# Kernel optimization log

Hardware: AMD Instinct MI355X
Metric: run time of the kernel (lower is better)

The kernel has to match this reference:

```python
import jax, jax.numpy as jnp
import numpy as np

B, S, H, I = 2, 1024, 1024, 4096
G, E = 4, 4
NE = G * E
CAP = 1024


def setup_inputs() -> dict:
    key = jax.random.key(0)
    ks = jax.random.split(key, 6)
    return {
        "hidden_states": jax.random.normal(ks[0], (B, S, H), jnp.float32),
        "group_router_w": jax.random.normal(ks[1], (G, H), jnp.float32) * 0.02,
        "expert_router_w": jax.random.normal(ks[2], (G, E, H), jnp.float32) * 0.02,
        "gate_w": jax.random.normal(ks[3], (NE, I, H), jnp.float32) * 0.02,
        "up_w": jax.random.normal(ks[4], (NE, I, H), jnp.float32) * 0.02,
        "down_w": jax.random.normal(ks[5], (NE, H, I), jnp.float32) * 0.02,
    }


def _forward(x, gw, erw, Wg, Wu, Wd):
    b, s, h = x.shape
    T = b * s
    xf = x.reshape(T, h)
    # level 1: group routing (fp32 softmax, top-2 groups)
    group_logits = xf @ gw.T                                        # [T,G]
    group_probs = jax.nn.softmax(group_logits.astype(jnp.float32), axis=-1)
    top_gp, top_gi = jax.lax.top_k(group_probs, 2)                  # [T,2]
    # level 2: per-group expert routing (top-1 expert within group)
    expert_logits = jnp.einsum('th,geh->tge', xf, erw)              # [T,G,E]
    expert_probs = jax.nn.softmax(expert_logits.astype(jnp.float32), axis=-1)
    e_idx = jnp.argmax(expert_probs, axis=-1)                       # [T,G]
    e_prob = jnp.max(expert_probs, axis=-1)                         # [T,G]
    sel_e = jnp.take_along_axis(e_idx, top_gi, axis=1)              # [T,2]
    sel_p = jnp.take_along_axis(e_prob, top_gi, axis=1)             # [T,2]
    eid = (top_gi * E + sel_e).reshape(-1)                          # [2T] global expert id
    wgt = (top_gp * sel_p).reshape(-1)                              # [2T] combine weight
    x2 = jnp.repeat(xf, 2, axis=0)                                  # [2T,H], slot-major per token
    # capacity-based dispatch: position within expert via cumsum of one-hot
    onehot = jax.nn.one_hot(eid, NE, dtype=jnp.int32)               # [2T,NE]
    pos = (jnp.cumsum(onehot, axis=0) * onehot).sum(axis=1) - 1     # [2T]
    keep = pos < CAP
    pos_c = jnp.where(keep, pos, CAP)                               # overflow -> dummy slot
    buf = jnp.zeros((NE, CAP + 1, h), x.dtype).at[eid, pos_c].set(x2)
    # grouped-GEMM gated FFN (SwiGLU) over all experts at once
    gate = jax.nn.silu(jnp.einsum('ech,eih->eci', buf, Wg))
    up = jnp.einsum('ech,eih->eci', buf, Wu)
    yexp = jnp.einsum('eci,ehi->ech', gate * up, Wd)                # [NE,CAP+1,H]
    # combine: gather back and weight; dropped tokens get zero weight
    y = yexp[eid, pos_c] * jnp.where(keep, wgt, 0.0)[:, None].astype(x.dtype)
    out = (y[0::2] + y[1::2]).reshape(b, s, h)
    aux_loss = jnp.zeros((), jnp.float32)  # aux-loss accumulation truncated in source; initialized to 0
    return out, aux_loss


def reference(hidden_states, group_router_w, expert_router_w, gate_w, up_w, down_w):
    return _forward(hidden_states, group_router_w, expert_router_w, gate_w, up_w, down_w)
```

## Files before the change

kernel.cpp:

```cpp
#include <hip/hip_runtime.h>
#include <hip/hip_bf16.h>

typedef float f32x4 __attribute__((ext_vector_type(4)));
typedef __bf16 bf16x8 __attribute__((ext_vector_type(8)));

#define H 1024
#define II 4096
#define NE 16
#define CAP 1024
#define NTOK 2048
#define NSLOT 4096

__global__ __launch_bounds__(256) void k_route(
    const float* __restrict__ x, const float* __restrict__ gw,
    const float* __restrict__ erw, int* __restrict__ eid,
    float* __restrict__ wgt) {
  int t = blockIdx.x * 4 + (threadIdx.x >> 6);
  int lane = threadIdx.x & 63;
  const float* xr = x + (size_t)t * H;
  double acc[20];
#pragma unroll
  for (int j = 0; j < 20; j++) acc[j] = 0.0;
  for (int it = 0; it < 16; ++it) {
    int h = it * 64 + lane;
    float xv = xr[h];
#pragma unroll
    for (int g = 0; g < 4; ++g) acc[g] += (double)xv * (double)gw[g * H + h];
#pragma unroll
    for (int j = 0; j < 16; ++j)
      acc[4 + j] += (double)xv * (double)erw[j * H + h];
  }
#pragma unroll
  for (int j = 0; j < 20; ++j) {
    double v = acc[j];
#pragma unroll
    for (int o = 32; o > 0; o >>= 1) v += __shfl_down(v, o, 64);
    acc[j] = v;
  }
  if (lane == 0) {
    float gl[4];
#pragma unroll
    for (int g = 0; g < 4; g++) gl[g] = (float)acc[g];
    int g1 = 0;
#pragma unroll
    for (int g = 1; g < 4; g++)
      if (gl[g] > gl[g1]) g1 = g;
    int g2 = (g1 == 0) ? 1 : 0;
#pragma unroll
    for (int g = 0; g < 4; g++)
      if (g != g1 && gl[g] > gl[g2]) g2 = g;
    float gm = fmaxf(fmaxf(gl[0], gl[1]), fmaxf(gl[2], gl[3]));
    float s = 0.f;
#pragma unroll
    for (int g = 0; g < 4; g++) s += expf(gl[g] - gm);
    float p[2] = {expf(gl[g1] - gm) / s, expf(gl[g2] - gm) / s};
    int gs[2] = {g1, g2};
#pragma unroll
    for (int k = 0; k < 2; k++) {
      int g = gs[k];
      float el[4];
#pragma unroll
      for (int e2 = 0; e2 < 4; e2++) el[e2] = (float)acc[4 + g * 4 + e2];
      int eb = 0;
#pragma unroll
      for (int e2 = 1; e2 < 4; e2++)
        if (el[e2] > el[eb]) eb = e2;
      float es = 0.f;
#pragma unroll
      for (int e2 = 0; e2 < 4; e2++) es += expf(el[e2] - el[eb]);
      eid[2 * t + k] = g * 4 + eb;
      wgt[2 * t + k] = p[k] * (1.f / es);
    }
  }
}

__global__ __launch_bounds__(1024) void k_scan(const int* __restrict__ eid,
                                               int* __restrict__ perm,
                                               int* __restrict__ cnt,
                                               int* __restrict__ kept) {
  int wid = threadIdx.x >> 6;
  int lane = threadIdx.x & 63;
  int base = 0;
  for (int it = 0; it < 64; ++it) {
    int slot = it * 64 + lane;
    int e = eid[slot];
    unsigned long long m = __ballot(e == wid);
    if (e == wid) {
      int pos = base + __popcll(m & ((1ull << lane) - 1ull));
      if (pos < CAP) {
        perm[wid * CAP + pos] = slot;
        kept[slot] = 1;
      } else {
        kept[slot] = 0;
      }
    }
    base += __popcll(m);
  }
  if (lane == 0) cnt[wid] = (base < CAP) ? base : CAP;
}

__global__ __launch_bounds__(256) void k_cvtx(const float* __restrict__ x,
                                              __bf16* __restrict__ xb) {
  size_t i = ((size_t)blockIdx.x * 256 + threadIdx.x) * 8;
  f32x4 a = *(const f32x4*)(x + i);
  f32x4 b = *(const f32x4*)(x + i + 4);
  bf16x8 o;
#pragma unroll
  for (int j = 0; j < 4; j++) {
    o[j] = (__bf16)a[j];
    o[j + 4] = (__bf16)b[j];
  }
  *(bf16x8*)(xb + i) = o;
}

#define FENCE_BAR()                                    \
  asm volatile("s_waitcnt lgkmcnt(0)" ::: "memory");   \
  __builtin_amdgcn_sched_barrier(0);                   \
  __builtin_amdgcn_s_barrier();

__global__ __launch_bounds__(256, 2) void k_gateup(
    const __bf16* __restrict__ xb, const float* __restrict__ Wg,
    const float* __restrict__ Wu, const int* __restrict__ perm,
    const int* __restrict__ cnt, __bf16* __restrict__ act) {
  __shared__ __bf16 As[2][128 * 64];
  __shared__ __bf16 Gs[2][64 * 64];
  __shared__ __bf16 Us[2][64 * 64];
  __shared__ int slotArr[128];
  const int e = blockIdx.z, nt = blockIdx.x, rt = blockIdx.y;
  const int ce = cnt[e];
  if (rt * 128 >= ce) return;
  const int tid = threadIdx.x, lane = tid & 63, wid = tid >> 6;
  if (tid < 128) {
    int ridx = rt * 128 + tid;
    slotArr[tid] = perm[e * CAP + (ridx < ce ? ridx : 0)];
  }
  __syncthreads();
  const int srow = tid >> 3;
  const int sch = tid & 7;
  const __bf16* pA[4];
  int wrA[4];
#pragma unroll
  for (int q = 0; q < 4; q++) {
    int r = q * 32 + srow;
    pA[q] = xb + (size_t)(slotArr[r] >> 1) * H + sch * 8;
    wrA[q] = r * 64 + (sch ^ (r & 7)) * 8;
  }
  const size_t ew = (size_t)e * II * H + (size_t)(nt * 64) * H;
  const float* pG[2];
  const float* pU[2];
  int wrW[2];
#pragma unroll
  for (int q = 0; q < 2; q++) {
    int r = q * 32 + srow;
    pG[q] = Wg + ew + (size_t)r * H + sch * 8;
    pU[q] = Wu + ew + (size_t)r * H + sch * 8;
    wrW[q] = r * 64 + (sch ^ (r & 7)) * 8;
  }
  const int wm = wid >> 1, wn = wid & 1;
  f32x4 accG[4][2], accU[4][2];
#pragma unroll
  for (int m = 0; m < 4; m++)
#pragma unroll
    for (int n = 0; n < 2; n++)
#pragma unroll
      for (int i = 0; i < 4; i++) {
        accG[m][n][i] = 0.f;
        accU[m][n][i] = 0.f;
      }
  bf16x8 a0[4], a1[4];
  f32x4 g00[2], g01[2], u00[2], u01[2];
  f32x4 g10[2], g11[2], u10[2], u11[2];

#define GU_LOADS(AS, G0, G1, U0, U1, T)                                    \
  {                                                                        \
    const int ko = (T) * 64;                                               \
    _Pragma("unroll") for (int q = 0; q < 4; q++)                          \
        AS[q] = *(const bf16x8*)(pA[q] + ko);                              \
    _Pragma("unroll") for (int q = 0; q < 2; q++) {                        \
      G0[q] = *(const f32x4*)(pG[q] + ko);                                 \
      G1[q] = *(const f32x4*)(pG[q] + ko + 4);                             \
      U0[q] = *(const f32x4*)(pU[q] + ko);                                 \
      U1[q] = *(const f32x4*)(pU[q] + ko + 4);                             \
    }                                                                      \
  }
#define GU_WRITE(BUF, AS, G0, G1, U0, U1)                                  \
  {                                                                        \
    _Pragma("unroll") for (int q = 0; q < 4; q++)                          \
        *(bf16x8*)&As[BUF][wrA[q]] = AS[q];                                \
    _Pragma("unroll") for (int q = 0; q < 2; q++) {                        \
      bf16x8 fg, fu;                                                       \
      _Pragma("unroll") for (int i = 0; i < 4; i++) {                      \
        fg[i] = (__bf16)G0[q][i];                                          \
        fg[i + 4] = (__bf16)G1[q][i];                                      \
        fu[i] = (__bf16)U0[q][i];                                          \
        fu[i + 4] = (__bf16)U1[q][i];                                      \
      }                                                                    \
      *(bf16x8*)&Gs[BUF][wrW[q]] = fg;                                     \
      *(bf16x8*)&Us[BUF][wrW[q]] = fu;                                     \
    }                                                                      \
  }
#define GU_COMPUTE(BUF)                                                    \
  {                                                                        \
    _Pragma("unroll") for (int kk = 0; kk < 2; ++kk) {                     \
      bf16x8 aF[4], gF[2], uF[2];                                          \
      _Pragma("unroll") for (int m = 0; m < 4; m++) {                      \
        int r = wm * 64 + m * 16 + (lane & 15);                            \
        int c = (kk * 4 + (lane >> 4)) ^ (r & 7);                          \
        aF[m] = *(const bf16x8*)&As[BUF][r * 64 + c * 8];                  \
      }                                                                    \
      _Pragma("unroll") for (int n = 0; n < 2; n++) {                      \
        int rg = wn * 32 + n * 16 + (lane & 15);                           \
        int c = (kk * 4 + (lane >> 4)) ^ (rg & 7);                         \
        gF[n] = *(const bf16x8*)&Gs[BUF][rg * 64 + c * 8];                 \
        uF[n] = *(const bf16x8*)&Us[BUF][rg * 64 + c * 8];                 \
      }                                                                    \
      _Pragma("unroll") for (int m = 0; m < 4; m++)                        \
          _Pragma("unroll") for (int n = 0; n < 2; n++) {                  \
        accG[m][n] = __builtin_amdgcn_mfma_f32_16x16x32_bf16(              \
            aF[m], gF[n], accG[m][n], 0, 0, 0);                            \
        accU[m][n] = __builtin_amdgcn_mfma_f32_16x16x32_bf16(              \
            aF[m], uF[n], accU[m][n], 0, 0, 0);                            \
      }                                                                    \
    }                                                                      \
  }

  GU_LOADS(a0, g00, g01, u00, u01, 0);
  GU_LOADS(a1, g10, g11, u10, u11, 1);
  GU_WRITE(0, a0, g00, g01, u00, u01);
  FENCE_BAR();
  for (int tt = 0; tt < 8; ++tt) {
    const int t0 = 2 * tt;
    if (t0 + 2 < 16) GU_LOADS(a0, g00, g01, u00, u01, t0 + 2);
    GU_COMPUTE(0);
    GU_WRITE(1, a1, g10, g11, u10, u11);
    FENCE_BAR();
    const int t1 = t0 + 1;
    if (t1 + 2 < 16) GU_LOADS(a1, g10, g11, u10, u11, t1 + 2);
    GU_COMPUTE(1);
    if (t1 + 1 < 16) {
      GU_WRITE(0, a0, g00, g01, u00, u01);
      FENCE_BAR();
    }
  }
  const int colB = nt * 64 + wn * 32;
#pragma unroll
  for (int m = 0; m < 4; m++)
#pragma unroll
    for (int n = 0; n < 2; n++)
#pragma unroll
      for (int i = 0; i < 4; i++) {
        int row = wm * 64 + m * 16 + (lane >> 4) * 4 + i;
        if (rt * 128 + row < ce) {
          int slot = slotArr[row];
          float g = accG[m][n][i];
          float u = accU[m][n][i];
          float a = (g / (1.f + __expf(-g))) * u;
          act[(size_t)slot * II + colB + n * 16 + (lane & 15)] = (__bf16)a;
        }
      }
}

__global__ __launch_bounds__(256, 2) void k_down(
    const __bf16* __restrict__ act, const float* __restrict__ Wd,
    const int* __restrict__ perm, const int* __restrict__ cnt,
    const float* __restrict__ wgt, float* __restrict__ y) {
  __shared__ __bf16 As[2][128 * 64];
  __shared__ __bf16 Ws[2][64 * 64];
  __shared__ int slotArr[128];
  const int e = blockIdx.z, nt = blockIdx.x, rt = blockIdx.y;
  const int ce = cnt[e];
  if (rt * 128 >= ce) return;
  const int tid = threadIdx.x, lane = tid & 63, wid = tid >> 6;
  if (tid < 128) {
    int ridx = rt * 128 + tid;
    slotArr[tid] = perm[e * CAP + (ridx < ce ? ridx : 0)];
  }
  __syncthreads();
  const int srow = tid >> 3;
  const int sch = tid & 7;
  const __bf16* pA[4];
  int wrA[4];
#pragma unroll
  for (int q = 0; q < 4; q++) {
    int r = q * 32 + srow;
    pA[q] = act + (size_t)slotArr[r] * II + sch * 8;
    wrA[q] = r * 64 + (sch ^ (r & 7)) * 8;
  }
  const float* pW[2];
  int wrW[2];
#pragma unroll
  for (int q = 0; q < 2; q++) {
    int r = q * 32 + srow;
    pW[q] = Wd + (size_t)e * H * II + (size_t)(nt * 64 + r) * II + sch * 8;
    wrW[q] = r * 64 + (sch ^ (r & 7)) * 8;
  }
  const int wm = wid >> 1, wn = wid & 1;
  f32x4 acc[4][2];
#pragma unroll
  for (int m = 0; m < 4; m++)
#pragma unroll
    for (int n = 0; n < 2; n++)
#pragma unroll
      for (int i = 0; i < 4; i++) acc[m][n][i] = 0.f;
  bf16x8 a0[4], a1[4];
  f32x4 w00[2], w01[2], w10[2], w11[2];

#define DN_LOADS(AS, W0, W1, T)                                            \
  {                                                                        \
    const int ko = (T) * 64;                                               \
    _Pragma("unroll") for (int q = 0; q < 4; q++)                          \
        AS[q] = *(const bf16x8*)(pA[q] + ko);                              \
    _Pragma("unroll") for (int q = 0; q < 2; q++) {                        \
      W0[q] = *(const f32x4*)(pW[q] + ko);                                 \
      W1[q] = *(const f32x4*)(pW[q] + ko + 4);                             \
    }                                                                      \
  }
#define DN_WRITE(BUF, AS, W0, W1)                                          \
  {                                                                        \
    _Pragma("unroll") for (int q = 0; q < 4; q++)                          \
        *(bf16x8*)&As[BUF][wrA[q]] = AS[q];                                \
    _Pragma("unroll") for (int q = 0; q < 2; q++) {                        \
      bf16x8 fw;                                                           \
      _Pragma("unroll") for (int i = 0; i < 4; i++) {                      \
        fw[i] = (__bf16)W0[q][i];                                          \
        fw[i + 4] = (__bf16)W1[q][i];                                      \
      }                                                                    \
      *(bf16x8*)&Ws[BUF][wrW[q]] = fw;                                     \
    }                                                                      \
  }
#define DN_COMPUTE(BUF)                                                    \
  {                                                                        \
    _Pragma("unroll") for (int kk = 0; kk < 2; ++kk) {                     \
      bf16x8 aF[4], wF[2];                                                 \
      _Pragma("unroll") for (int m = 0; m < 4; m++) {                      \
        int r = wm * 64 + m * 16 + (lane & 15);                            \
        int c = (kk * 4 + (lane >> 4)) ^ (r & 7);                          \
        aF[m] = *(const bf16x8*)&As[BUF][r * 64 + c * 8];                  \
      }                                                                    \
      _Pragma("unroll") for (int n = 0; n < 2; n++) {                      \
        int rw = wn * 32 + n * 16 + (lane & 15);                           \
        int c = (kk * 4 + (lane >> 4)) ^ (rw & 7);                         \
        wF[n] = *(const bf16x8*)&Ws[BUF][rw * 64 + c * 8];                 \
      }                                                                    \
      _Pragma("unroll") for (int m = 0; m < 4; m++)                        \
          _Pragma("unroll") for (int n = 0; n < 2; n++)                    \
              acc[m][n] = __builtin_amdgcn_mfma_f32_16x16x32_bf16(         \
                  aF[m], wF[n], acc[m][n], 0, 0, 0);                       \
    }                                                                      \
  }

  DN_LOADS(a0, w00, w01, 0);
  DN_LOADS(a1, w10, w11, 1);
  DN_WRITE(0, a0, w00, w01);
  FENCE_BAR();
  for (int tt = 0; tt < 32; ++tt) {
    const int t0 = 2 * tt;
    if (t0 + 2 < 64) DN_LOADS(a0, w00, w01, t0 + 2);
    DN_COMPUTE(0);
    DN_WRITE(1, a1, w10, w11);
    FENCE_BAR();
    const int t1 = t0 + 1;
    if (t1 + 2 < 64) DN_LOADS(a1, w10, w11, t1 + 2);
    DN_COMPUTE(1);
    if (t1 + 1 < 64) {
      DN_WRITE(0, a0, w00, w01);
      FENCE_BAR();
    }
  }
  const int colB = nt * 64 + wn * 32;
#pragma unroll
  for (int m = 0; m < 4; m++)
#pragma unroll
    for (int n = 0; n < 2; n++)
#pragma unroll
      for (int i = 0; i < 4; i++) {
        int row = wm * 64 + m * 16 + (lane >> 4) * 4 + i;
        if (rt * 128 + row < ce) {
          int slot = slotArr[row];
          y[(size_t)slot * H + colB + n * 16 + (lane & 15)] =
              wgt[slot] * acc[m][n][i];
        }
      }
}

__global__ __launch_bounds__(256) void k_combine(const float* __restrict__ y,
                                                 const int* __restrict__ kept,
                                                 float* __restrict__ out) {
  int t = blockIdx.x, tid = threadIdx.x;
  const f32x4* y0 = (const f32x4*)(y + (size_t)(2 * t) * H);
  const f32x4* y1 = (const f32x4*)(y + (size_t)(2 * t + 1) * H);
  f32x4 a, b;
#pragma unroll
  for (int i = 0; i < 4; i++) {
    a[i] = 0.f;
    b[i] = 0.f;
  }
  if (kept[2 * t]) a = y0[tid];
  if (kept[2 * t + 1]) b = y1[tid];
  ((f32x4*)out)[(size_t)t * 256 + tid] = a + b;
  if (t == 0 && tid == 0) out[(size_t)NTOK * H] = 0.f;
}

extern "C" void kernel_launch(void* const* d_in, const int* in_sizes, int n_in,
                              void* d_out, int out_size, void* d_ws,
                              size_t ws_size, hipStream_t stream) {
  const float* x = (const float*)d_in[0];
  const float* gw = (const float*)d_in[1];
  const float* erw = (const float*)d_in[2];
  const float* Wg = (const float*)d_in[3];
  const float* Wu = (const float*)d_in[4];
  const float* Wd = (const float*)d_in[5];
  float* out = (float*)d_out;
  char* ws = (char*)d_ws;
  int* eid = (int*)(ws);
  float* wgt = (float*)(ws + (16 << 10));
  int* kept = (int*)(ws + (32 << 10));
  int* cnt = (int*)(ws + (48 << 10));
  int* perm = (int*)(ws + (64 << 10));
  __bf16* act = (__bf16*)(ws + (128 << 10));
  float* yb = (float*)(ws + (128 << 10) + (size_t)NSLOT * II * 2);
  __bf16* xb = (__bf16*)(ws + (128 << 10) + (size_t)NSLOT * II * 2 +
                         (size_t)NSLOT * H * 4);

  k_route<<<NTOK / 4, 256, 0, stream>>>(x, gw, erw, eid, wgt);
  k_scan<<<1, 1024, 0, stream>>>(eid, perm, cnt, kept);
  k_cvtx<<<NTOK * H / 8 / 256, 256, 0, stream>>>(x, xb);
  k_gateup<<<dim3(64, 8, 16), 256, 0, stream>>>(xb, Wg, Wu, perm, cnt, act);
  k_down<<<dim3(16, 8, 16), 256, 0, stream>>>(act, Wd, perm, cnt, wgt, yb);
  k_combine<<<NTOK, 256, 0, stream>>>(yb, kept, out);
}
```

Before: 372.5 us.

## Widen expert GEMM tiles to 128x128 with 512-thread single-buffered LDS blocks

Both the gate/up and down grouped GEMMs move from 256-thread blocks with 128x64 output tiles to 512-thread blocks (eight waves) with 128x128 tiles. The grid's N dimension is halved to match. LDS drops from double-buffered to a single buffer refilled from register-prefetched data, with extra barriers around each write. The gate/up K-step shrinks to 32. The aim is to halve redundant reloads of the gathered activation rows and raise work per block. In exchange the kernels synchronise more often and get less LDS overlap, while traffic on the fp32 weights, which likely dominates, is unchanged.

```diff
diff --git a/kernel.cpp b/kernel.cpp
--- a/kernel.cpp
+++ b/kernel.cpp
@@ -118,13 +118,13 @@
   __builtin_amdgcn_sched_barrier(0);                   \
   __builtin_amdgcn_s_barrier();
 
-__global__ __launch_bounds__(256, 2) void k_gateup(
+__global__ __launch_bounds__(512, 2) void k_gateup(
     const __bf16* __restrict__ xb, const float* __restrict__ Wg,
     const float* __restrict__ Wu, const int* __restrict__ perm,
     const int* __restrict__ cnt, __bf16* __restrict__ act) {
-  __shared__ __bf16 As[2][128 * 64];
-  __shared__ __bf16 Gs[2][64 * 64];
-  __shared__ __bf16 Us[2][64 * 64];
+  __shared__ __bf16 As[128 * 32];
+  __shared__ __bf16 Gs[128 * 32];
+  __shared__ __bf16 Us[128 * 32];
   __shared__ int slotArr[128];
   const int e = blockIdx.z, nt = blockIdx.x, rt = blockIdx.y;
   const int ce = cnt[e];
@@ -135,121 +135,99 @@
     slotArr[tid] = perm[e * CAP + (ridx < ce ? ridx : 0)];
   }
   __syncthreads();
-  const int srow = tid >> 3;
-  const int sch = tid & 7;
-  const __bf16* pA[4];
-  int wrA[4];
-#pragma unroll
-  for (int q = 0; q < 4; q++) {
-    int r = q * 32 + srow;
-    pA[q] = xb + (size_t)(slotArr[r] >> 1) * H + sch * 8;
-    wrA[q] = r * 64 + (sch ^ (r & 7)) * 8;
-  }
-  const size_t ew = (size_t)e * II * H + (size_t)(nt * 64) * H;
-  const float* pG[2];
-  const float* pU[2];
-  int wrW[2];
-#pragma unroll
-  for (int q = 0; q < 2; q++) {
-    int r = q * 32 + srow;
-    pG[q] = Wg + ew + (size_t)r * H + sch * 8;
-    pU[q] = Wu + ew + (size_t)r * H + sch * 8;
-    wrW[q] = r * 64 + (sch ^ (r & 7)) * 8;
-  }
+  const int srow = tid >> 2;
+  const int sch = tid & 3;
+  const int wrOff = srow * 32 + (sch ^ ((srow >> 1) & 3)) * 8;
+  const __bf16* pA = xb + (size_t)(slotArr[srow] >> 1) * H + sch * 8;
+  const size_t ew = (size_t)e * II * H + (size_t)(nt * 128 + srow) * H;
+  const float* pG = Wg + ew + sch * 8;
+  const float* pU = Wu + ew + sch * 8;
   const int wm = wid >> 1, wn = wid & 1;
-  f32x4 accG[4][2], accU[4][2];
-#pragma unroll
-  for (int m = 0; m < 4; m++)
-#pragma unroll
-    for (int n = 0; n < 2; n++)
+  f32x4 accG[2][4], accU[2][4];
+#pragma unroll
+  for (int m = 0; m < 2; m++)
+#pragma unroll
+    for (int n = 0; n < 4; n++)
 #pragma unroll
       for (int i = 0; i < 4; i++) {
         accG[m][n][i] = 0.f;
         accU[m][n][i] = 0.f;
       }
-  bf16x8 a0[4], a1[4];
-  f32x4 g00[2], g01[2], u00[2], u01[2];
-  f32x4 g10[2], g11[2], u10[2], u11[2];
-
-#define GU_LOADS(AS, G0, G1, U0, U1, T)                                    \
-  {                                                                        \
-    const int ko = (T) * 64;                                               \
-    _Pragma("unroll") for (int q = 0; q < 4; q++)                          \
-        AS[q] = *(const bf16x8*)(pA[q] + ko);                              \
-    _Pragma("unroll") for (int q = 0; q < 2; q++) {                        \
-      G0[q] = *(const f32x4*)(pG[q] + ko);                                 \
-      G1[q] = *(const f32x4*)(pG[q] + ko + 4);                             \
-      U0[q] = *(const f32x4*)(pU[q] + ko);                                 \
-      U1[q] = *(const f32x4*)(pU[q] + ko + 4);                             \
-    }                                                                      \
-  }
-#define GU_WRITE(BUF, AS, G0, G1, U0, U1)                                  \
-  {                                                                        \
-    _Pragma("unroll") for (int q = 0; q < 4; q++)                          \
-        *(bf16x8*)&As[BUF][wrA[q]] = AS[q];                                \
-    _Pragma("unroll") for (int q = 0; q < 2; q++) {                        \
-      bf16x8 fg, fu;                                                       \
-      _Pragma("unroll") for (int i = 0; i < 4; i++) {                      \
-        fg[i] = (__bf16)G0[q][i];                                          \
-        fg[i + 4] = (__bf16)G1[q][i];                                      \
-        fu[i] = (__bf16)U0[q][i];                                          \
-        fu[i + 4] = (__bf16)U1[q][i];                                      \
-      }                                                                    \
-      *(bf16x8*)&Gs[BUF][wrW[q]] = fg;                                     \
-      *(bf16x8*)&Us[BUF][wrW[q]] = fu;                                     \
-    }                                                                      \
-  }
-#define GU_COMPUTE(BUF)                                                    \
-  {                                                                        \
-    _Pragma("unroll") for (int kk = 0; kk < 2; ++kk) {                     \
-      bf16x8 aF[4], gF[2], uF[2];                                          \
-      _Pragma("unroll") for (int m = 0; m < 4; m++) {                      \
-        int r = wm * 64 + m * 16 + (lane & 15);                            \
-        int c = (kk * 4 + (lane >> 4)) ^ (r & 7);                          \
-        aF[m] = *(const bf16x8*)&As[BUF][r * 64 + c * 8];                  \
-      }                                                                    \
-      _Pragma("unroll") for (int n = 0; n < 2; n++) {                      \
-        int rg = wn * 32 + n * 16 + (lane & 15);                           \
-        int c = (kk * 4 + (lane >> 4)) ^ (rg & 7);                         \
-        gF[n] = *(const bf16x8*)&Gs[BUF][rg * 64 + c * 8];                 \
-        uF[n] = *(const bf16x8*)&Us[BUF][rg * 64 + c * 8];                 \
-      }                                                                    \
-      _Pragma("unroll") for (int m = 0; m < 4; m++)                        \
-          _Pragma("unroll") for (int n = 0; n < 2; n++) {                  \
-        accG[m][n] = __builtin_amdgcn_mfma_f32_16x16x32_bf16(              \
-            aF[m], gF[n], accG[m][n], 0, 0, 0);                            \
-        accU[m][n] = __builtin_amdgcn_mfma_f32_16x16x32_bf16(              \
-            aF[m], uF[n], accU[m][n], 0, 0, 0);                            \
-      }                                                                    \
-    }                                                                      \
-  }
-
-  GU_LOADS(a0, g00, g01, u00, u01, 0);
-  GU_LOADS(a1, g10, g11, u10, u11, 1);
-  GU_WRITE(0, a0, g00, g01, u00, u01);
+  bf16x8 sA0, sA1;
+  f32x4 sG00, sG01, sU00, sU01, sG10, sG11, sU10, sU11;
+
+#define GU_LOADS(A8, G0, G1, U0, U1, T)     \
+  {                                         \
+    const int ko = (T) * 32;                \
+    A8 = *(const bf16x8*)(pA + ko);         \
+    G0 = *(const f32x4*)(pG + ko);          \
+    G1 = *(const f32x4*)(pG + ko + 4);      \
+    U0 = *(const f32x4*)(pU + ko);          \
+    U1 = *(const f32x4*)(pU + ko + 4);      \
+  }
+#define GU_WRITE(A8, G0, G1, U0, U1)        \
+  {                                         \
+    *(bf16x8*)&As[wrOff] = A8;              \
+    bf16x8 fg, fu;                          \
+    _Pragma("unroll") for (int i = 0; i < 4; i++) { \
+      fg[i] = (__bf16)G0[i];                \
+      fg[i + 4] = (__bf16)G1[i];            \
+      fu[i] = (__bf16)U0[i];                \
+      fu[i + 4] = (__bf16)U1[i];            \
+    }                                       \
+    *(bf16x8*)&Gs[wrOff] = fg;              \
+    *(bf16x8*)&Us[wrOff] = fu;              \
+  }
+#define GU_COMPUTE()                                                     \
+  {                                                                      \
+    bf16x8 aF[2], gF[4], uF[4];                                          \
+    _Pragma("unroll") for (int m = 0; m < 2; m++) {                      \
+      int r = wm * 32 + m * 16 + (lane & 15);                            \
+      int c = (lane >> 4) ^ ((r >> 1) & 3);                              \
+      aF[m] = *(const bf16x8*)&As[r * 32 + c * 8];                       \
+    }                                                                    \
+    _Pragma("unroll") for (int n = 0; n < 4; n++) {                      \
+      int r = wn * 64 + n * 16 + (lane & 15);                            \
+      int c = (lane >> 4) ^ ((r >> 1) & 3);                              \
+      gF[n] = *(const bf16x8*)&Gs[r * 32 + c * 8];                       \
+      uF[n] = *(const bf16x8*)&Us[r * 32 + c * 8];                       \
+    }                                                                    \
+    _Pragma("unroll") for (int m = 0; m < 2; m++)                        \
+        _Pragma("unroll") for (int n = 0; n < 4; n++) {                  \
+      accG[m][n] = __builtin_amdgcn_mfma_f32_16x16x32_bf16(              \
+          aF[m], gF[n], accG[m][n], 0, 0, 0);                            \
+      accU[m][n] = __builtin_amdgcn_mfma_f32_16x16x32_bf16(              \
+          aF[m], uF[n], accU[m][n], 0, 0, 0);                            \
+    }                                                                    \
+  }
+
+  GU_LOADS(sA0, sG00, sG01, sU00, sU01, 0);
+  GU_LOADS(sA1, sG10, sG11, sU10, sU11, 1);
+  GU_WRITE(sA0, sG00, sG01, sU00, sU01);
   FENCE_BAR();
-  for (int tt = 0; tt < 8; ++tt) {
+  for (int tt = 0; tt < 16; ++tt) {
     const int t0 = 2 * tt;
-    if (t0 + 2 < 16) GU_LOADS(a0, g00, g01, u00, u01, t0 + 2);
-    GU_COMPUTE(0);
-    GU_WRITE(1, a1, g10, g11, u10, u11);
+    if (t0 + 2 < 32) GU_LOADS(sA0, sG00, sG01, sU00, sU01, t0 + 2);
+    GU_COMPUTE();
     FENCE_BAR();
-    const int t1 = t0 + 1;
-    if (t1 + 2 < 16) GU_LOADS(a1, g10, g11, u10, u11, t1 + 2);
-    GU_COMPUTE(1);
-    if (t1 + 1 < 16) {
-      GU_WRITE(0, a0, g00, g01, u00, u01);
+    GU_WRITE(sA1, sG10, sG11, sU10, sU11);
+    FENCE_BAR();
+    if (t0 + 3 < 32) GU_LOADS(sA1, sG10, sG11, sU10, sU11, t0 + 3);
+    GU_COMPUTE();
+    if (t0 + 2 < 32) {
+      FENCE_BAR();
+      GU_WRITE(sA0, sG00, sG01, sU00, sU01);
       FENCE_BAR();
     }
   }
-  const int colB = nt * 64 + wn * 32;
-#pragma unroll
-  for (int m = 0; m < 4; m++)
-#pragma unroll
-    for (int n = 0; n < 2; n++)
+  const int colB = nt * 128 + wn * 64;
+#pragma unroll
+  for (int m = 0; m < 2; m++)
+#pragma unroll
+    for (int n = 0; n < 4; n++)
 #pragma unroll
       for (int i = 0; i < 4; i++) {
-        int row = wm * 64 + m * 16 + (lane >> 4) * 4 + i;
+        int row = wm * 32 + m * 16 + (lane >> 4) * 4 + i;
         if (rt * 128 + row < ce) {
           int slot = slotArr[row];
           float g = accG[m][n][i];
@@ -260,12 +238,12 @@
       }
 }
 
-__global__ __launch_bounds__(256, 2) void k_down(
+__global__ __launch_bounds__(512, 2) void k_down(
     const __bf16* __restrict__ act, const float* __restrict__ Wd,
     const int* __restrict__ perm, const int* __restrict__ cnt,
     const float* __restrict__ wgt, float* __restrict__ y) {
-  __shared__ __bf16 As[2][128 * 64];
-  __shared__ __bf16 Ws[2][64 * 64];
+  __shared__ __bf16 As[128 * 64];
+  __shared__ __bf16 Ws[128 * 64];
   __shared__ int slotArr[128];
   const int e = blockIdx.z, nt = blockIdx.x, rt = blockIdx.y;
   const int ce = cnt[e];
@@ -276,105 +254,96 @@
     slotArr[tid] = perm[e * CAP + (ridx < ce ? ridx : 0)];
   }
   __syncthreads();
-  const int srow = tid >> 3;
-  const int sch = tid & 7;
-  const __bf16* pA[4];
-  int wrA[4];
-#pragma unroll
-  for (int q = 0; q < 4; q++) {
-    int r = q * 32 + srow;
-    pA[q] = act + (size_t)slotArr[r] * II + sch * 8;
-    wrA[q] = r * 64 + (sch ^ (r & 7)) * 8;
-  }
-  const float* pW[2];
-  int wrW[2];
-#pragma unroll
-  for (int q = 0; q < 2; q++) {
-    int r = q * 32 + srow;
-    pW[q] = Wd + (size_t)e * H * II + (size_t)(nt * 64 + r) * II + sch * 8;
-    wrW[q] = r * 64 + (sch ^ (r & 7)) * 8;
-  }
+  const int srow = tid >> 2;
+  const int c0 = tid & 3;
+  const int wr0 = srow * 64 + (c0 ^ (srow & 7)) * 8;
+  const int wr1 = srow * 64 + ((c0 + 4) ^ (srow & 7)) * 8;
+  const __bf16* pA = act + (size_t)slotArr[srow] * II + c0 * 8;
+  const float* pW =
+      Wd + (size_t)e * H * II + (size_t)(nt * 128 + srow) * II + c0 * 8;
   const int wm = wid >> 1, wn = wid & 1;
-  f32x4 acc[4][2];
-#pragma unroll
-  for (int m = 0; m < 4; m++)
-#pragma unroll
-    for (int n = 0; n < 2; n++)
+  f32x4 acc[2][4];
+#pragma unroll
+  for (int m = 0; m < 2; m++)
+#pragma unroll
+    for (int n = 0; n < 4; n++)
 #pragma unroll
       for (int i = 0; i < 4; i++) acc[m][n][i] = 0.f;
-  bf16x8 a0[4], a1[4];
-  f32x4 w00[2], w01[2], w10[2], w11[2];
-
-#define DN_LOADS(AS, W0, W1, T)                                            \
-  {                                                                        \
-    const int ko = (T) * 64;                                               \
-    _Pragma("unroll") for (int q = 0; q < 4; q++)                          \
-        AS[q] = *(const bf16x8*)(pA[q] + ko);                              \
-    _Pragma("unroll") for (int q = 0; q < 2; q++) {                        \
-      W0[q] = *(const f32x4*)(pW[q] + ko);                                 \
-      W1[q] = *(const f32x4*)(pW[q] + ko + 4);                             \
-    }                                                                      \
-  }
-#define DN_WRITE(BUF, AS, W0, W1)                                          \
-  {                                                                        \
-    _Pragma("unroll") for (int q = 0; q < 4; q++)                          \
-        *(bf16x8*)&As[BUF][wrA[q]] = AS[q];                                \
-    _Pragma("unroll") for (int q = 0; q < 2; q++) {                        \
-      bf16x8 fw;                                                           \
-      _Pragma("unroll") for (int i = 0; i < 4; i++) {                      \
-        fw[i] = (__bf16)W0[q][i];                                          \
-        fw[i + 4] = (__bf16)W1[q][i];                                      \
-      }                                                                    \
-      *(bf16x8*)&Ws[BUF][wrW[q]] = fw;                                     \
-    }                                                                      \
-  }
-#define DN_COMPUTE(BUF)                                                    \
-  {                                                                        \
-    _Pragma("unroll") for (int kk = 0; kk < 2; ++kk) {                     \
-      bf16x8 aF[4], wF[2];                                                 \
-      _Pragma("unroll") for (int m = 0; m < 4; m++) {                      \
-        int r = wm * 64 + m * 16 + (lane & 15);                            \
-        int c = (kk * 4 + (lane >> 4)) ^ (r & 7);                          \
-        aF[m] = *(const bf16x8*)&As[BUF][r * 64 + c * 8];                  \
-      }                                                                    \
-      _Pragma("unroll") for (int n = 0; n < 2; n++) {                      \
-        int rw = wn * 32 + n * 16 + (lane & 15);                           \
-        int c = (kk * 4 + (lane >> 4)) ^ (rw & 7);                         \
-        wF[n] = *(const bf16x8*)&Ws[BUF][rw * 64 + c * 8];                 \
-      }                                                                    \
-      _Pragma("unroll") for (int m = 0; m < 4; m++)                        \
-          _Pragma("unroll") for (int n = 0; n < 2; n++)                    \
-              acc[m][n] = __builtin_amdgcn_mfma_f32_16x16x32_bf16(         \
-                  aF[m], wF[n], acc[m][n], 0, 0, 0);                       \
-    }                                                                      \
-  }
-
-  DN_LOADS(a0, w00, w01, 0);
-  DN_LOADS(a1, w10, w11, 1);
-  DN_WRITE(0, a0, w00, w01);
+  bf16x8 dA00, dA01, dA10, dA11;
+  f32x4 dW000, dW001, dW010, dW011, dW100, dW101, dW110, dW111;
+
+#define DN_LOADS(A0, A1, W00, W01, W10, W11, T) \
+  {                                             \
+    const int ko = (T) * 64;                    \
+    A0 = *(const bf16x8*)(pA + ko);             \
+    A1 = *(const bf16x8*)(pA + ko + 32);        \
+    W00 = *(const f32x4*)(pW + ko);             \
+    W01 = *(const f32x4*)(pW + ko + 4);         \
+    W10 = *(const f32x4*)(pW + ko + 32);        \
+    W11 = *(const f32x4*)(pW + ko + 36);        \
+  }
+#define DN_WRITE(A0, A1, W00, W01, W10, W11)    \
+  {                                             \
+    *(bf16x8*)&As[wr0] = A0;                    \
+    *(bf16x8*)&As[wr1] = A1;                    \
+    bf16x8 f0, f1;                              \
+    _Pragma("unroll") for (int i = 0; i < 4; i++) { \
+      f0[i] = (__bf16)W00[i];                   \
+      f0[i + 4] = (__bf16)W01[i];               \
+      f1[i] = (__bf16)W10[i];                   \
+      f1[i + 4] = (__bf16)W11[i];               \
+    }                                           \
+    *(bf16x8*)&Ws[wr0] = f0;                    \
+    *(bf16x8*)&Ws[wr1] = f1;                    \
+  }
+#define DN_COMPUTE()                                                     \
+  {                                                                      \
+    _Pragma("unroll") for (int kk = 0; kk < 2; ++kk) {                   \
+      bf16x8 aF[2], wF[4];                                               \
+      _Pragma("unroll") for (int m = 0; m < 2; m++) {                    \
+        int r = wm * 32 + m * 16 + (lane & 15);                          \
+        int c = (kk * 4 + (lane >> 4)) ^ (r & 7);                        \
+        aF[m] = *(const bf16x8*)&As[r * 64 + c * 8];                     \
+      }                                                                  \
+      _Pragma("unroll") for (int n = 0; n < 4; n++) {                    \
+        int r = wn * 64 + n * 16 + (lane & 15);                          \
+        int c = (kk * 4 + (lane >> 4)) ^ (r & 7);                        \
+        wF[n] = *(const bf16x8*)&Ws[r * 64 + c * 8];                     \
+      }                                                                  \
+      _Pragma("unroll") for (int m = 0; m < 2; m++)                      \
+          _Pragma("unroll") for (int n = 0; n < 4; n++)                  \
+              acc[m][n] = __builtin_amdgcn_mfma_f32_16x16x32_bf16(       \
+                  aF[m], wF[n], acc[m][n], 0, 0, 0);                     \
+    }                                                                    \
+  }
+
+  DN_LOADS(dA00, dA01, dW000, dW001, dW010, dW011, 0);
+  DN_LOADS(dA10, dA11, dW100, dW101, dW110, dW111, 1);
+  DN_WRITE(dA00, dA01, dW000, dW001, dW010, dW011);
   FENCE_BAR();
   for (int tt = 0; tt < 32; ++tt) {
     const int t0 = 2 * tt;
-    if (t0 + 2 < 64) DN_LOADS(a0, w00, w01, t0 + 2);
-    DN_COMPUTE(0);
-    DN_WRITE(1, a1, w10, w11);
+    if (t0 + 2 < 64) DN_LOADS(dA00, dA01, dW000, dW001, dW010, dW011, t0 + 2);
+    DN_COMPUTE();
     FENCE_BAR();
-    const int t1 = t0 + 1;
-    if (t1 + 2 < 64) DN_LOADS(a1, w10, w11, t1 + 2);
-    DN_COMPUTE(1);
-    if (t1 + 1 < 64) {
-      DN_WRITE(0, a0, w00, w01);
+    DN_WRITE(dA10, dA11, dW100, dW101, dW110, dW111);
+    FENCE_BAR();
+    if (t0 + 3 < 64) DN_LOADS(dA10, dA11, dW100, dW101, dW110, dW111, t0 + 3);
+    DN_COMPUTE();
+    if (t0 + 2 < 64) {
+      FENCE_BAR();
+      DN_WRITE(dA00, dA01, dW000, dW001, dW010, dW011);
       FENCE_BAR();
     }
   }
-  const int colB = nt * 64 + wn * 32;
-#pragma unroll
-  for (int m = 0; m < 4; m++)
-#pragma unroll
-    for (int n = 0; n < 2; n++)
+  const int colB = nt * 128 + wn * 64;
+#pragma unroll
+  for (int m = 0; m < 2; m++)
+#pragma unroll
+    for (int n = 0; n < 4; n++)
 #pragma unroll
       for (int i = 0; i < 4; i++) {
-        int row = wm * 64 + m * 16 + (lane >> 4) * 4 + i;
+        int row = wm * 32 + m * 16 + (lane >> 4) * 4 + i;
         if (rt * 128 + row < ce) {
           int slot = slotArr[row];
           y[(size_t)slot * H + colB + n * 16 + (lane & 15)] =
@@ -425,7 +394,7 @@
   k_route<<<NTOK / 4, 256, 0, stream>>>(x, gw, erw, eid, wgt);
   k_scan<<<1, 1024, 0, stream>>>(eid, perm, cnt, kept);
   k_cvtx<<<NTOK * H / 8 / 256, 256, 0, stream>>>(x, xb);
-  k_gateup<<<dim3(64, 8, 16), 256, 0, stream>>>(xb, Wg, Wu, perm, cnt, act);
-  k_down<<<dim3(16, 8, 16), 256, 0, stream>>>(act, Wd, perm, cnt, wgt, yb);
+  k_gateup<<<dim3(32, 8, 16), 512, 0, stream>>>(xb, Wg, Wu, perm, cnt, act);
+  k_down<<<dim3(8, 8, 16), 512, 0, stream>>>(act, Wd, perm, cnt, wgt, yb);
   k_combine<<<NTOK, 256, 0, stream>>>(yb, kept, out);
 }
```

Measured after the change: 371.8 us. No clear change (-0.2%).
